# Kernel tuning notes

Hardware: AMD Instinct MI355X
Metric: run time of the kernel (lower is better)

The kernel has to match this reference:

```python
import jax, jax.numpy as jnp
import numpy as np


def setup_inputs() -> dict:
    key = jax.random.key(0)
    k0, k1, k2, k3, k4, k5 = jax.random.split(key, 6)
    L1, L2, B, D = 512, 512, 32, 1024
    inputs1 = jax.random.normal(k0, (L1, B, D), dtype=jnp.float32)
    inputs2 = jax.random.normal(k1, (L2, B, D), dtype=jnp.float32)
    # mask value 0 marks a valid token (module keeps pairs where both masks == 0)
    mask1 = jax.random.randint(k2, (L1, B), 0, 2, dtype=jnp.int64)
    mask2 = jax.random.randint(k3, (L2, B), 0, 2, dtype=jnp.int64)
    W = jax.random.normal(k4, (D, D), dtype=jnp.float32) * 0.02
    b = jax.random.normal(k5, (1,), dtype=jnp.float32) * 0.02
    return {"inputs1": inputs1, "inputs2": inputs2, "mask1": mask1,
            "mask2": mask2, "W": W, "b": b, "k": 256}


def reference(inputs1, inputs2, mask1, mask2, W, b, k):
    # inputs: [len, bsz, hdim]; masks: [len, bsz]
    H1 = jnp.transpose(inputs1, (1, 0, 2))  # [B, L1, D]
    H2 = jnp.transpose(inputs2, (1, 0, 2))  # [B, L2, D]
    # bilinear scores: H1 @ W @ H2^T + b, then relu  -> [B, L1, L2]
    S = jax.nn.relu(jnp.einsum('bid,de,bje->bij', H1, W, H2) + b[0])
    # pair is valid iff both mask entries are 0
    valid = (mask1.T[:, :, None] == 0) & (mask2.T[:, None, :] == 0)  # [B, L1, L2]
    B = S.shape[0]
    S_flat = jnp.where(valid.reshape(B, -1), S.reshape(B, -1), -jnp.inf)
    num_elems = S_flat.shape[1]
    k_actual = min(k, num_elems)
    q, _ = jax.lax.top_k(S_flat, k_actual)  # [B, k_actual]
    # replace -inf tail entries with the last finite value in each row
    neg = jnp.isneginf(q)
    q_num_finite = k_actual - neg.sum(axis=-1)  # [B]
    fill = jnp.take_along_axis(q, (q_num_finite - 1)[:, None], axis=1)  # [B, 1]
    q = jnp.where(neg, fill, q)
    if k_actual < k:
        q = jnp.concatenate(
            [q, jnp.broadcast_to(q[:, -1:], (B, k - k_actual))], axis=1)
    return q
```

## Files before the change

kernel.cpp:

```cpp
#include <hip/hip_runtime.h>

typedef __bf16 bf16_t;
typedef bf16_t bf16x8 __attribute__((ext_vector_type(8)));
typedef float floatx4 __attribute__((ext_vector_type(4)));

#define L1C 512
#define L2C 512
#define BC  32
#define DC  1024
#define KTOP 256
#define NBIN 4096
#define CAP  1024
#define FBUF 16384

__device__ __forceinline__ unsigned short f2bf(float f) {
    unsigned u = __float_as_uint(f);
    u += 0x7FFFu + ((u >> 16) & 1u);
    return (unsigned short)(u >> 16);
}

__device__ __forceinline__ void g2l16(const unsigned short* g, unsigned short* l) {
    __builtin_amdgcn_global_load_lds((const unsigned int*)g, (unsigned int*)l,
                                     16, 0, 0);
}

__device__ __forceinline__ float decode_key(unsigned k) {
    return __uint_as_float(k & 0x7FFFFFFFu);
}

__global__ __launch_bounds__(512) void scan_kernel(
    const int* __restrict__ mask1, const int* __restrict__ mask2,
    int* __restrict__ idx1, int* __restrict__ idx2,
    unsigned* __restrict__ nv1, unsigned* __restrict__ nv2,
    unsigned* __restrict__ cnt) {
    __shared__ unsigned sc[512];
    int b = blockIdx.x, t = threadIdx.x;
    for (int which = 0; which < 2; which++) {
        const int* m = which ? mask2 : mask1;
        int* idx = which ? idx2 : idx1;
        unsigned v = (m[t * BC + b] == 0) ? 1u : 0u;
        sc[t] = v;
        __syncthreads();
        for (int off = 1; off < 512; off <<= 1) {
            unsigned x = (t >= off) ? sc[t - off] : 0u;
            __syncthreads();
            sc[t] += x;
            __syncthreads();
        }
        if (v) idx[b * 512 + sc[t] - 1] = t;
        if (t == 511) { if (which) nv2[b] = sc[511]; else nv1[b] = sc[511]; }
        __syncthreads();
    }
    if (t < 16) cnt[b * 16 + t] = 0;
}

__global__ __launch_bounds__(256) void prep_kernel(
    const float* __restrict__ in1, const float* __restrict__ in2,
    const float* __restrict__ W,
    const int* __restrict__ idx1, const int* __restrict__ idx2,
    const unsigned* __restrict__ nv1, const unsigned* __restrict__ nv2,
    unsigned short* __restrict__ A1c, unsigned short* __restrict__ A2c,
    unsigned short* __restrict__ Wb) {
    int r = blockIdx.x, t = threadIdx.x;
    const float* src;
    unsigned short* dst;
    if (r < 2 * 16384) {
        int which = r >> 14;
        int rr = r & 16383;
        int b = rr >> 9, vi = rr & 511;
        unsigned nv = which ? nv2[b] : nv1[b];
        unsigned pad = (nv + 127u) & ~127u;
        if ((unsigned)vi >= pad) return;
        dst = (which ? A2c : A1c) + ((size_t)b * 512 + vi) * DC;
        if ((unsigned)vi < nv) {
            int l = (which ? idx2 : idx1)[b * 512 + vi];
            src = (which ? in2 : in1) + (size_t)(l * BC + b) * DC;
        } else {
            ushort4 z = {0, 0, 0, 0};
            reinterpret_cast<ushort4*>(dst)[t] = z;
            return;
        }
    } else {
        int r3 = r - 2 * 16384;
        src = W + (size_t)r3 * DC;
        dst = Wb + (size_t)r3 * DC;
    }
    float4 v = reinterpret_cast<const float4*>(src)[t];
    ushort4 o;
    o.x = f2bf(v.x); o.y = f2bf(v.y); o.z = f2bf(v.z); o.w = f2bf(v.w);
    reinterpret_cast<ushort4*>(dst)[t] = o;
}

__global__ __launch_bounds__(256) void gemm1_kernel(
    const unsigned short* __restrict__ A,
    const unsigned short* __restrict__ Bt,
    unsigned short* __restrict__ C,
    const unsigned* __restrict__ nv2) {
    int bi = blockIdx.x >> 2, mt = blockIdx.x & 3;
    unsigned pad2 = (nv2[bi] + 127u) & ~127u;
    if ((unsigned)(mt * 128) >= pad2) return;
    __shared__ unsigned short As[128][32];
    __shared__ unsigned short Bs[128][32];
    int tid = threadIdx.x;
    int wave = tid >> 6, lane = tid & 63;
    int lane15 = lane & 15, quad = lane >> 4;
    int wm = wave >> 1, wn = wave & 1;
    size_t m0 = (size_t)bi * 512 + mt * 128;
    size_t n0 = (size_t)blockIdx.y * 128;

    floatx4 zero = {0.f, 0.f, 0.f, 0.f};
    floatx4 acc[4][4];
#pragma unroll
    for (int i = 0; i < 4; i++)
#pragma unroll
        for (int j = 0; j < 4; j++) acc[i][j] = zero;

    for (int k0 = 0; k0 < DC; k0 += 32) {
#pragma unroll
        for (int c = 0; c < 2; c++) {
            int cid = c * 256 + tid;
            int row = cid >> 2, col8 = (cid & 3) * 8;
            unsigned short* lbase = &As[0][0] + (c * 256 + wave * 64) * 8;
            g2l16(&A[(m0 + row) * DC + k0 + col8], lbase);
            unsigned short* lbase2 = &Bs[0][0] + (c * 256 + wave * 64) * 8;
            g2l16(&Bt[(n0 + row) * DC + k0 + col8], lbase2);
        }
        __syncthreads();
        bf16x8 af[4], bfr[4];
#pragma unroll
        for (int mi = 0; mi < 4; mi++)
            af[mi] = *reinterpret_cast<const bf16x8*>(&As[wm * 64 + mi * 16 + lane15][quad * 8]);
#pragma unroll
        for (int ni = 0; ni < 4; ni++)
            bfr[ni] = *reinterpret_cast<const bf16x8*>(&Bs[wn * 64 + ni * 16 + lane15][quad * 8]);
#pragma unroll
        for (int mi = 0; mi < 4; mi++)
#pragma unroll
            for (int ni = 0; ni < 4; ni++)
                acc[mi][ni] = __builtin_amdgcn_mfma_f32_16x16x32_bf16(
                    af[mi], bfr[ni], acc[mi][ni], 0, 0, 0);
        __syncthreads();
    }
#pragma unroll
    for (int mi = 0; mi < 4; mi++)
#pragma unroll
        for (int ni = 0; ni < 4; ni++)
#pragma unroll
            for (int r = 0; r < 4; r++) {
                size_t row = m0 + wm * 64 + mi * 16 + quad * 4 + r;
                size_t col = n0 + wn * 64 + ni * 16 + lane15;
                C[row * DC + col] = f2bf(acc[mi][ni][r]);
            }
}

__global__ __launch_bounds__(256) void gemm2_kernel(
    const unsigned short* __restrict__ A1c,
    const unsigned short* __restrict__ V,
    const unsigned* __restrict__ nv1, const unsigned* __restrict__ nv2,
    const float* __restrict__ bptr,
    unsigned* __restrict__ cand,
    unsigned* __restrict__ cnt) {
    int L = blockIdx.x;
    int xcd = L & 7, tile = (L >> 3) & 15, chunk = L >> 7;
    int b = xcd + (chunk << 3);
    int bx = tile & 3, by = tile >> 2;
    int m0 = bx * 128, n0 = by * 128;
    int gblk = b * 16 + by * 4 + bx;
    int tid = threadIdx.x;
    unsigned nv1v = nv1[b], nv2v = nv2[b];
    unsigned pad1 = (nv1v + 127u) & ~127u, pad2 = (nv2v + 127u) & ~127u;
    if ((unsigned)m0 >= pad1 || (unsigned)n0 >= pad2) {
        if (tid == 0) cnt[gblk] = 0;
        return;
    }
    __shared__ unsigned short As[128][32];
    __shared__ unsigned short Bs[128][32];
    __shared__ unsigned lh[NBIN];
    __shared__ unsigned csum[256];
    __shared__ unsigned tsh, lcnt, zeq;
    int wave = tid >> 6, lane = tid & 63;
    int lane15 = lane & 15, quad = lane >> 4;
    int wm = wave >> 1, wn = wave & 1;
    const unsigned short* Ab = A1c + (size_t)b * 512 * DC;
    const unsigned short* Bb = V + (size_t)b * 512 * DC;

    for (int i = tid; i < NBIN; i += 256) lh[i] = 0;

    floatx4 zero = {0.f, 0.f, 0.f, 0.f};
    floatx4 acc[4][4];
#pragma unroll
    for (int i = 0; i < 4; i++)
#pragma unroll
        for (int j = 0; j < 4; j++) acc[i][j] = zero;

    for (int k0 = 0; k0 < DC; k0 += 32) {
#pragma unroll
        for (int c = 0; c < 2; c++) {
            int cid = c * 256 + tid;
            int row = cid >> 2, col8 = (cid & 3) * 8;
            unsigned short* lbase = &As[0][0] + (c * 256 + wave * 64) * 8;
            g2l16(&Ab[(size_t)(m0 + row) * DC + k0 + col8], lbase);
            unsigned short* lbase2 = &Bs[0][0] + (c * 256 + wave * 64) * 8;
            g2l16(&Bb[(size_t)(n0 + row) * DC + k0 + col8], lbase2);
        }
        __syncthreads();
        bf16x8 af[4], bfr[4];
#pragma unroll
        for (int mi = 0; mi < 4; mi++)
            af[mi] = *reinterpret_cast<const bf16x8*>(&As[wm * 64 + mi * 16 + lane15][quad * 8]);
#pragma unroll
        for (int ni = 0; ni < 4; ni++)
            bfr[ni] = *reinterpret_cast<const bf16x8*>(&Bs[wn * 64 + ni * 16 + lane15][quad * 8]);
#pragma unroll
        for (int mi = 0; mi < 4; mi++)
#pragma unroll
            for (int ni = 0; ni < 4; ni++)
                acc[mi][ni] = __builtin_amdgcn_mfma_f32_16x16x32_bf16(
                    af[mi], bfr[ni], acc[mi][ni], 0, 0, 0);
        __syncthreads();
    }

    float bias = bptr[0];
    unsigned zc = 0;
#pragma unroll
    for (int ni = 0; ni < 4; ni++) {
        int jl = n0 + wn * 64 + ni * 16 + lane15;
        int v2 = (unsigned)jl < nv2v;
#pragma unroll
        for (int mi = 0; mi < 4; mi++)
#pragma unroll
            for (int r = 0; r < 4; r++) {
                int il = m0 + wm * 64 + mi * 16 + quad * 4 + r;
                float s = acc[mi][ni][r] + bias;
                if (v2 && (unsigned)il < nv1v) {
                    if (s > 0.f)
                        atomicAdd(&lh[(__float_as_uint(s) | 0x80000000u) >> 20], 1u);
                    else
                        zc++;
                }
            }
    }
    if (zc) atomicAdd(&lh[2048], zc);
    __syncthreads();
    unsigned s16 = 0;
#pragma unroll
    for (int i = 0; i < 16; i++) s16 += lh[tid * 16 + i];
    csum[tid] = s16;
    __syncthreads();
    if (tid == 0) {
        unsigned cum = 0, bin = 2048;
        int found = 0;
        for (int c = 255; c >= 128 && !found; --c) {
            unsigned cs = csum[c];
            if (cum + cs >= KTOP) {
                for (int bb = c * 16 + 15; bb >= c * 16; --bb) {
                    unsigned h = lh[bb];
                    if (cum + h >= KTOP) { bin = (unsigned)bb; found = 1; break; }
                    cum += h;
                }
            } else cum += cs;
        }
        tsh = bin << 20;
        lcnt = 0;
        zeq = 0;
    }
    __syncthreads();
    unsigned T = tsh;
    unsigned base = (unsigned)gblk * CAP;
#pragma unroll
    for (int ni = 0; ni < 4; ni++) {
        int jl = n0 + wn * 64 + ni * 16 + lane15;
        int v2 = (unsigned)jl < nv2v;
#pragma unroll
        for (int mi = 0; mi < 4; mi++)
#pragma unroll
            for (int r = 0; r < 4; r++) {
                int il = m0 + wm * 64 + mi * 16 + quad * 4 + r;
                float s = acc[mi][ni][r] + bias;
                s = s > 0.f ? s : 0.f;
                unsigned key = (v2 && (unsigned)il < nv1v)
                                   ? (__float_as_uint(s) | 0x80000000u) : 0u;
                if (key > T) {
                    unsigned p = atomicAdd(&lcnt, 1u);
                    if (p < CAP) cand[base + p] = key;
                } else if (key == T) {
                    unsigned z = atomicAdd(&zeq, 1u);
                    if (z < KTOP) {
                        unsigned p = atomicAdd(&lcnt, 1u);
                        if (p < CAP) cand[base + p] = key;
                    }
                }
            }
    }
    __syncthreads();
    if (tid == 0) cnt[gblk] = lcnt < CAP ? lcnt : CAP;
}

__global__ __launch_bounds__(1024) void final_kernel(
    const unsigned* __restrict__ cand, const unsigned* __restrict__ cnt,
    float* __restrict__ out) {
    __shared__ unsigned buf[FBUF];
    __shared__ unsigned h[NBIN];
    __shared__ unsigned ss[256];
    __shared__ unsigned scnt_s[16], off_s[16];
    __shared__ unsigned ntot_s, sel_c, sel_a, B_s, R_s, mcount;
    __shared__ int have_s;
    __shared__ unsigned srt[256];
    int b = blockIdx.x, tid = threadIdx.x;
    int wv = tid >> 6, ln = tid & 63;

    if (tid < 16) {
        unsigned c = cnt[b * 16 + tid];
        scnt_s[tid] = c < CAP ? c : CAP;
    }
    __syncthreads();
    if (tid == 0) {
        unsigned o = 0;
        for (int i = 0; i < 16; i++) { off_s[i] = o; o += scnt_s[i]; }
        ntot_s = o;
        have_s = 1;
    }
    __syncthreads();
    {
        unsigned c = scnt_s[wv], o = off_s[wv];
        const unsigned* p = cand + (size_t)(b * 16 + wv) * CAP;
        for (unsigned i = ln; i < c; i += 64) buf[o + i] = p[i];
    }
    __syncthreads();
    unsigned n = ntot_s;

    unsigned Kr = KTOP;
    unsigned pfx = 0;
    unsigned kth = 0;
    for (int pass = 0; pass < 3; pass++) {
        int bins = (pass < 2) ? NBIN : 256;
        int shift = (pass == 0) ? 20 : (pass == 1) ? 8 : 0;
        int nch = bins >> 4;
        for (int i = tid; i < bins; i += 1024) h[i] = 0;
        __syncthreads();
        for (unsigned i = tid; i < n; i += 1024) {
            unsigned k = buf[i];
            bool ok = (pass == 0) ||
                      (pass == 1 && (k >> 20) == pfx) ||
                      (pass == 2 && (k >> 8) == pfx);
            if (ok) atomicAdd(&h[(k >> shift) & (bins - 1)], 1u);
        }
        __syncthreads();
        if (tid < nch) {
            unsigned s = 0;
#pragma unroll
            for (int i = 0; i < 16; i++) s += h[tid * 16 + i];
            ss[tid] = s;
        }
        __syncthreads();
        for (int off = 1; off < nch; off <<= 1) {
            unsigned v = 0;
            if (tid < nch && tid + (unsigned)off < (unsigned)nch) v = ss[tid + off];
            __syncthreads();
            if (tid < nch) ss[tid] += v;
            __syncthreads();
        }
        if (pass == 0) {
            if (tid == 0) have_s = (ss[0] >= KTOP);
            __syncthreads();
            if (!have_s) break;
        }
        if (tid < nch) {
            unsigned above = (tid + 1 < (unsigned)nch) ? ss[tid + 1] : 0u;
            if (above < Kr && ss[tid] >= Kr) { sel_c = tid; sel_a = above; }
        }
        __syncthreads();
        if (tid == 0) {
            unsigned cum = sel_a;
            for (int bb = (int)sel_c * 16 + 15; bb >= (int)sel_c * 16; --bb) {
                unsigned hb = h[bb];
                if (cum + hb >= Kr) { B_s = (unsigned)bb; R_s = Kr - cum; break; }
                cum += hb;
            }
        }
        __syncthreads();
        unsigned Bv = B_s;
        Kr = R_s;
        if (pass == 0) pfx = Bv;
        else if (pass == 1) pfx = (pfx << 12) | Bv;
        else kth = (pfx << 8) | Bv;
        __syncthreads();
    }

    if (tid == 0) mcount = 0;
    __syncthreads();
    int have = have_s;
    unsigned lim = have ? kth : 0u;
    for (unsigned i = tid; i < n; i += 1024) {
        unsigned k = buf[i];
        if (k > lim) {
            unsigned p = atomicAdd(&mcount, 1u);
            if (p < 256) srt[p] = k;
        }
    }
    __syncthreads();
    unsigned m = mcount;
    if (tid < 256 && tid >= (int)m) srt[tid] = have ? kth : 0u;
    for (int k2 = 2; k2 <= 256; k2 <<= 1) {
        for (int j2 = k2 >> 1; j2 > 0; j2 >>= 1) {
            __syncthreads();
            if (tid < 256) {
                int ixj = tid ^ j2;
                if (ixj > tid) {
                    unsigned a = srt[tid], c = srt[ixj];
                    bool up = (tid & k2) == 0;
                    if (up ? (a < c) : (a > c)) { srt[tid] = c; srt[ixj] = a; }
                }
            }
        }
    }
    __syncthreads();
    if (tid < 256) {
        unsigned nval = have ? KTOP : (m < KTOP ? m : KTOP);
        float v;
        if ((unsigned)tid < nval) v = decode_key(srt[tid]);
        else v = (nval > 0) ? decode_key(srt[nval - 1]) : -__builtin_inff();
        out[b * KTOP + tid] = v;
    }
}

extern "C" void kernel_launch(void* const* d_in, const int* in_sizes, int n_in,
                              void* d_out, int out_size, void* d_ws, size_t ws_size,
                              hipStream_t stream) {
    const float* in1   = (const float*)d_in[0];
    const float* in2   = (const float*)d_in[1];
    const int*   mask1 = (const int*)d_in[2];
    const int*   mask2 = (const int*)d_in[3];
    const float* W     = (const float*)d_in[4];
    const float* bias  = (const float*)d_in[5];
    float* out = (float*)d_out;

    char* ws = (char*)d_ws;
    size_t off = 0;
    const size_t nElem = (size_t)512 * BC * DC;
    unsigned short* A1c = (unsigned short*)(ws + off); off += nElem * 2;
    unsigned short* A2c = (unsigned short*)(ws + off); off += nElem * 2;
    unsigned short* Wb  = (unsigned short*)(ws + off); off += (size_t)DC * DC * 2;
    unsigned short* V   = (unsigned short*)(ws + off); off += nElem * 2;
    unsigned* cand = (unsigned*)(ws + off); off += (size_t)BC * 16 * CAP * 4;
    unsigned* cnt  = (unsigned*)(ws + off); off += (size_t)BC * 16 * 4;
    int* idx1 = (int*)(ws + off); off += (size_t)BC * 512 * 4;
    int* idx2 = (int*)(ws + off); off += (size_t)BC * 512 * 4;
    unsigned* nv1 = (unsigned*)(ws + off); off += BC * 4;
    unsigned* nv2 = (unsigned*)(ws + off); off += BC * 4;

    scan_kernel<<<BC, 512, 0, stream>>>(mask1, mask2, idx1, idx2, nv1, nv2, cnt);
    prep_kernel<<<2 * 16384 + 1024, 256, 0, stream>>>(
        in1, in2, W, idx1, idx2, nv1, nv2, A1c, A2c, Wb);
    gemm1_kernel<<<dim3(128, 8), 256, 0, stream>>>(A2c, Wb, V, nv2);
    gemm2_kernel<<<512, 256, 0, stream>>>(A1c, V, nv1, nv2, bias, cand, cnt);
    final_kernel<<<BC, 1024, 0, stream>>>(cand, cnt, out);
}
```

Baseline: 263.2 us.

## Shrink GEMM tiles to 64 rows and pad valid tokens to 64

Both GEMMs now use smaller tiles: 64x128 in gemm1 and 64x64 in gemm2. Valid-token padding drops from 128 to 64, which wastes less compute on padded rows and launches more blocks, so occupancy rises and the CU load is more even. gemm2 now emits 64 candidate segments per batch with a smaller cap. Its per-block threshold search uses a parallel suffix scan instead of a serial thread-0 loop, and final_kernel clamps the total candidate count to its buffer. Smaller tiles lower data reuse per MFMA and mean more histogram clears and per-block overhead.

```diff
diff --git a/kernel.cpp b/kernel.cpp
--- a/kernel.cpp
+++ b/kernel.cpp
@@ -10,7 +10,8 @@
 #define DC  1024
 #define KTOP 256
 #define NBIN 4096
-#define CAP  1024
+#define CAP  512
+#define NT   64
 #define FBUF 16384
 
 __device__ __forceinline__ unsigned short f2bf(float f) {
@@ -51,7 +52,7 @@
         if (t == 511) { if (which) nv2[b] = sc[511]; else nv1[b] = sc[511]; }
         __syncthreads();
     }
-    if (t < 16) cnt[b * 16 + t] = 0;
+    if (t < NT) cnt[b * NT + t] = 0;
 }
 
 __global__ __launch_bounds__(256) void prep_kernel(
@@ -69,7 +70,7 @@
         int rr = r & 16383;
         int b = rr >> 9, vi = rr & 511;
         unsigned nv = which ? nv2[b] : nv1[b];
-        unsigned pad = (nv + 127u) & ~127u;
+        unsigned pad = (nv + 63u) & ~63u;
         if ((unsigned)vi >= pad) return;
         dst = (which ? A2c : A1c) + ((size_t)b * 512 + vi) * DC;
         if ((unsigned)vi < nv) {
@@ -96,47 +97,50 @@
     const unsigned short* __restrict__ Bt,
     unsigned short* __restrict__ C,
     const unsigned* __restrict__ nv2) {
-    int bi = blockIdx.x >> 2, mt = blockIdx.x & 3;
-    unsigned pad2 = (nv2[bi] + 127u) & ~127u;
-    if ((unsigned)(mt * 128) >= pad2) return;
-    __shared__ unsigned short As[128][32];
+    int bi = blockIdx.x >> 3, mt = blockIdx.x & 7;
+    unsigned pad2 = (nv2[bi] + 63u) & ~63u;
+    if ((unsigned)(mt * 64) >= pad2) return;
+    __shared__ unsigned short As[64][32];
     __shared__ unsigned short Bs[128][32];
     int tid = threadIdx.x;
     int wave = tid >> 6, lane = tid & 63;
     int lane15 = lane & 15, quad = lane >> 4;
-    int wm = wave >> 1, wn = wave & 1;
-    size_t m0 = (size_t)bi * 512 + mt * 128;
+    size_t m0 = (size_t)bi * 512 + mt * 64;
     size_t n0 = (size_t)blockIdx.y * 128;
 
     floatx4 zero = {0.f, 0.f, 0.f, 0.f};
-    floatx4 acc[4][4];
+    floatx4 acc[4][2];
 #pragma unroll
     for (int i = 0; i < 4; i++)
 #pragma unroll
-        for (int j = 0; j < 4; j++) acc[i][j] = zero;
+        for (int j = 0; j < 2; j++) acc[i][j] = zero;
 
     for (int k0 = 0; k0 < DC; k0 += 32) {
+        {
+            int row = tid >> 2, col8 = (tid & 3) * 8;
+            g2l16(&A[(m0 + row) * DC + k0 + col8],
+                  &As[0][0] + (wave * 64) * 8);
+        }
 #pragma unroll
         for (int c = 0; c < 2; c++) {
-            int cid = c * 256 + tid;
-            int row = cid >> 2, col8 = (cid & 3) * 8;
-            unsigned short* lbase = &As[0][0] + (c * 256 + wave * 64) * 8;
-            g2l16(&A[(m0 + row) * DC + k0 + col8], lbase);
-            unsigned short* lbase2 = &Bs[0][0] + (c * 256 + wave * 64) * 8;
-            g2l16(&Bt[(n0 + row) * DC + k0 + col8], lbase2);
-        }
-        __syncthreads();
-        bf16x8 af[4], bfr[4];
+            int cid2 = c * 256 + tid;
+            int row = cid2 >> 2, col8 = (cid2 & 3) * 8;
+            g2l16(&Bt[(n0 + row) * DC + k0 + col8],
+                  &Bs[0][0] + (c * 256 + wave * 64) * 8);
+        }
+        __syncthreads();
+        bf16x8 af[4], bfr[2];
 #pragma unroll
         for (int mi = 0; mi < 4; mi++)
-            af[mi] = *reinterpret_cast<const bf16x8*>(&As[wm * 64 + mi * 16 + lane15][quad * 8]);
-#pragma unroll
-        for (int ni = 0; ni < 4; ni++)
-            bfr[ni] = *reinterpret_cast<const bf16x8*>(&Bs[wn * 64 + ni * 16 + lane15][quad * 8]);
+            af[mi] = *reinterpret_cast<const bf16x8*>(&As[mi * 16 + lane15][quad * 8]);
+#pragma unroll
+        for (int ni = 0; ni < 2; ni++)
+            bfr[ni] = *reinterpret_cast<const bf16x8*>(
+                &Bs[wave * 32 + ni * 16 + lane15][quad * 8]);
 #pragma unroll
         for (int mi = 0; mi < 4; mi++)
 #pragma unroll
-            for (int ni = 0; ni < 4; ni++)
+            for (int ni = 0; ni < 2; ni++)
                 acc[mi][ni] = __builtin_amdgcn_mfma_f32_16x16x32_bf16(
                     af[mi], bfr[ni], acc[mi][ni], 0, 0, 0);
         __syncthreads();
@@ -144,11 +148,11 @@
 #pragma unroll
     for (int mi = 0; mi < 4; mi++)
 #pragma unroll
-        for (int ni = 0; ni < 4; ni++)
+        for (int ni = 0; ni < 2; ni++)
 #pragma unroll
             for (int r = 0; r < 4; r++) {
-                size_t row = m0 + wm * 64 + mi * 16 + quad * 4 + r;
-                size_t col = n0 + wn * 64 + ni * 16 + lane15;
+                size_t row = m0 + mi * 16 + quad * 4 + r;
+                size_t col = n0 + wave * 32 + ni * 16 + lane15;
                 C[row * DC + col] = f2bf(acc[mi][ni][r]);
             }
 }
@@ -161,62 +165,52 @@
     unsigned* __restrict__ cand,
     unsigned* __restrict__ cnt) {
     int L = blockIdx.x;
-    int xcd = L & 7, tile = (L >> 3) & 15, chunk = L >> 7;
+    int xcd = L & 7, tile = (L >> 3) & 63, chunk = L >> 9;
     int b = xcd + (chunk << 3);
-    int bx = tile & 3, by = tile >> 2;
-    int m0 = bx * 128, n0 = by * 128;
-    int gblk = b * 16 + by * 4 + bx;
+    int tx = tile & 7, ty = tile >> 3;
+    int m0 = ty * 64, n0 = tx * 64;
+    int gblk = b * NT + tile;
     int tid = threadIdx.x;
     unsigned nv1v = nv1[b], nv2v = nv2[b];
-    unsigned pad1 = (nv1v + 127u) & ~127u, pad2 = (nv2v + 127u) & ~127u;
+    unsigned pad1 = (nv1v + 63u) & ~63u, pad2 = (nv2v + 63u) & ~63u;
     if ((unsigned)m0 >= pad1 || (unsigned)n0 >= pad2) {
         if (tid == 0) cnt[gblk] = 0;
         return;
     }
-    __shared__ unsigned short As[128][32];
-    __shared__ unsigned short Bs[128][32];
+    __shared__ unsigned short As[64][32];
+    __shared__ unsigned short Bs[64][32];
     __shared__ unsigned lh[NBIN];
     __shared__ unsigned csum[256];
-    __shared__ unsigned tsh, lcnt, zeq;
+    __shared__ unsigned sel_c, sel_a, tsh, lcnt, zeq;
     int wave = tid >> 6, lane = tid & 63;
     int lane15 = lane & 15, quad = lane >> 4;
-    int wm = wave >> 1, wn = wave & 1;
     const unsigned short* Ab = A1c + (size_t)b * 512 * DC;
     const unsigned short* Bb = V + (size_t)b * 512 * DC;
 
     for (int i = tid; i < NBIN; i += 256) lh[i] = 0;
+    if (tid == 0) { sel_c = 0xFFFFFFFFu; lcnt = 0; zeq = 0; }
 
     floatx4 zero = {0.f, 0.f, 0.f, 0.f};
-    floatx4 acc[4][4];
-#pragma unroll
-    for (int i = 0; i < 4; i++)
-#pragma unroll
-        for (int j = 0; j < 4; j++) acc[i][j] = zero;
+    floatx4 acc[4];
+#pragma unroll
+    for (int i = 0; i < 4; i++) acc[i] = zero;
 
     for (int k0 = 0; k0 < DC; k0 += 32) {
-#pragma unroll
-        for (int c = 0; c < 2; c++) {
-            int cid = c * 256 + tid;
-            int row = cid >> 2, col8 = (cid & 3) * 8;
-            unsigned short* lbase = &As[0][0] + (c * 256 + wave * 64) * 8;
-            g2l16(&Ab[(size_t)(m0 + row) * DC + k0 + col8], lbase);
-            unsigned short* lbase2 = &Bs[0][0] + (c * 256 + wave * 64) * 8;
-            g2l16(&Bb[(size_t)(n0 + row) * DC + k0 + col8], lbase2);
-        }
-        __syncthreads();
-        bf16x8 af[4], bfr[4];
-#pragma unroll
-        for (int mi = 0; mi < 4; mi++)
-            af[mi] = *reinterpret_cast<const bf16x8*>(&As[wm * 64 + mi * 16 + lane15][quad * 8]);
+        int row = tid >> 2, col8 = (tid & 3) * 8;
+        g2l16(&Ab[(size_t)(m0 + row) * DC + k0 + col8],
+              &As[0][0] + (wave * 64) * 8);
+        g2l16(&Bb[(size_t)(n0 + row) * DC + k0 + col8],
+              &Bs[0][0] + (wave * 64) * 8);
+        __syncthreads();
+        bf16x8 af, bfr[4];
+        af = *reinterpret_cast<const bf16x8*>(&As[wave * 16 + lane15][quad * 8]);
 #pragma unroll
         for (int ni = 0; ni < 4; ni++)
-            bfr[ni] = *reinterpret_cast<const bf16x8*>(&Bs[wn * 64 + ni * 16 + lane15][quad * 8]);
-#pragma unroll
-        for (int mi = 0; mi < 4; mi++)
-#pragma unroll
-            for (int ni = 0; ni < 4; ni++)
-                acc[mi][ni] = __builtin_amdgcn_mfma_f32_16x16x32_bf16(
-                    af[mi], bfr[ni], acc[mi][ni], 0, 0, 0);
+            bfr[ni] = *reinterpret_cast<const bf16x8*>(&Bs[ni * 16 + lane15][quad * 8]);
+#pragma unroll
+        for (int ni = 0; ni < 4; ni++)
+            acc[ni] = __builtin_amdgcn_mfma_f32_16x16x32_bf16(
+                af, bfr[ni], acc[ni], 0, 0, 0);
         __syncthreads();
     }
 
@@ -224,21 +218,19 @@
     unsigned zc = 0;
 #pragma unroll
     for (int ni = 0; ni < 4; ni++) {
-        int jl = n0 + wn * 64 + ni * 16 + lane15;
+        int jl = n0 + ni * 16 + lane15;
         int v2 = (unsigned)jl < nv2v;
 #pragma unroll
-        for (int mi = 0; mi < 4; mi++)
-#pragma unroll
-            for (int r = 0; r < 4; r++) {
-                int il = m0 + wm * 64 + mi * 16 + quad * 4 + r;
-                float s = acc[mi][ni][r] + bias;
-                if (v2 && (unsigned)il < nv1v) {
-                    if (s > 0.f)
-                        atomicAdd(&lh[(__float_as_uint(s) | 0x80000000u) >> 20], 1u);
-                    else
-                        zc++;
-                }
-            }
+        for (int r = 0; r < 4; r++) {
+            int il = m0 + wave * 16 + quad * 4 + r;
+            float s = acc[ni][r] + bias;
+            if (v2 && (unsigned)il < nv1v) {
+                if (s > 0.f)
+                    atomicAdd(&lh[(__float_as_uint(s) | 0x80000000u) >> 20], 1u);
+                else
+                    zc++;
+            }
+        }
     }
     if (zc) atomicAdd(&lh[2048], zc);
     __syncthreads();
@@ -247,50 +239,57 @@
     for (int i = 0; i < 16; i++) s16 += lh[tid * 16 + i];
     csum[tid] = s16;
     __syncthreads();
+    for (int off = 1; off < 256; off <<= 1) {
+        unsigned v = (tid + off < 256) ? csum[tid + off] : 0u;
+        __syncthreads();
+        csum[tid] += v;
+        __syncthreads();
+    }
+    {
+        unsigned above = (tid < 255) ? csum[tid + 1] : 0u;
+        if (tid >= 128 && csum[tid] >= KTOP && above < KTOP) {
+            sel_c = (unsigned)tid; sel_a = above;
+        }
+    }
+    __syncthreads();
     if (tid == 0) {
-        unsigned cum = 0, bin = 2048;
-        int found = 0;
-        for (int c = 255; c >= 128 && !found; --c) {
-            unsigned cs = csum[c];
-            if (cum + cs >= KTOP) {
-                for (int bb = c * 16 + 15; bb >= c * 16; --bb) {
-                    unsigned h = lh[bb];
-                    if (cum + h >= KTOP) { bin = (unsigned)bb; found = 1; break; }
-                    cum += h;
-                }
-            } else cum += cs;
-        }
-        tsh = bin << 20;
-        lcnt = 0;
-        zeq = 0;
+        if (sel_c == 0xFFFFFFFFu) {
+            tsh = 2048u << 20;
+        } else {
+            unsigned cum = sel_a, bin = 2048;
+            for (int bb = (int)sel_c * 16 + 15; bb >= (int)sel_c * 16; --bb) {
+                unsigned hb = lh[bb];
+                if (cum + hb >= KTOP) { bin = (unsigned)bb; break; }
+                cum += hb;
+            }
+            tsh = bin << 20;
+        }
     }
     __syncthreads();
     unsigned T = tsh;
     unsigned base = (unsigned)gblk * CAP;
 #pragma unroll
     for (int ni = 0; ni < 4; ni++) {
-        int jl = n0 + wn * 64 + ni * 16 + lane15;
+        int jl = n0 + ni * 16 + lane15;
         int v2 = (unsigned)jl < nv2v;
 #pragma unroll
-        for (int mi = 0; mi < 4; mi++)
-#pragma unroll
-            for (int r = 0; r < 4; r++) {
-                int il = m0 + wm * 64 + mi * 16 + quad * 4 + r;
-                float s = acc[mi][ni][r] + bias;
-                s = s > 0.f ? s : 0.f;
-                unsigned key = (v2 && (unsigned)il < nv1v)
-                                   ? (__float_as_uint(s) | 0x80000000u) : 0u;
-                if (key > T) {
+        for (int r = 0; r < 4; r++) {
+            int il = m0 + wave * 16 + quad * 4 + r;
+            float s = acc[ni][r] + bias;
+            s = s > 0.f ? s : 0.f;
+            unsigned key = (v2 && (unsigned)il < nv1v)
+                               ? (__float_as_uint(s) | 0x80000000u) : 0u;
+            if (key > T) {
+                unsigned p = atomicAdd(&lcnt, 1u);
+                if (p < CAP) cand[base + p] = key;
+            } else if (key == T) {
+                unsigned z = atomicAdd(&zeq, 1u);
+                if (z < KTOP) {
                     unsigned p = atomicAdd(&lcnt, 1u);
                     if (p < CAP) cand[base + p] = key;
-                } else if (key == T) {
-                    unsigned z = atomicAdd(&zeq, 1u);
-                    if (z < KTOP) {
-                        unsigned p = atomicAdd(&lcnt, 1u);
-                        if (p < CAP) cand[base + p] = key;
-                    }
                 }
             }
+        }
     }
     __syncthreads();
     if (tid == 0) cnt[gblk] = lcnt < CAP ? lcnt : CAP;
@@ -302,28 +301,34 @@
     __shared__ unsigned buf[FBUF];
     __shared__ unsigned h[NBIN];
     __shared__ unsigned ss[256];
-    __shared__ unsigned scnt_s[16], off_s[16];
+    __shared__ unsigned scnt_s[NT], off_s[NT];
     __shared__ unsigned ntot_s, sel_c, sel_a, B_s, R_s, mcount;
     __shared__ int have_s;
     __shared__ unsigned srt[256];
     int b = blockIdx.x, tid = threadIdx.x;
     int wv = tid >> 6, ln = tid & 63;
 
-    if (tid < 16) {
-        unsigned c = cnt[b * 16 + tid];
+    if (tid < NT) {
+        unsigned c = cnt[b * NT + tid];
         scnt_s[tid] = c < CAP ? c : CAP;
     }
     __syncthreads();
     if (tid == 0) {
         unsigned o = 0;
-        for (int i = 0; i < 16; i++) { off_s[i] = o; o += scnt_s[i]; }
+        for (int i = 0; i < NT; i++) {
+            unsigned c = scnt_s[i];
+            if (o + c > FBUF) c = (o < FBUF) ? FBUF - o : 0;
+            scnt_s[i] = c;
+            off_s[i] = o;
+            o += c;
+        }
         ntot_s = o;
         have_s = 1;
     }
     __syncthreads();
-    {
-        unsigned c = scnt_s[wv], o = off_s[wv];
-        const unsigned* p = cand + (size_t)(b * 16 + wv) * CAP;
+    for (int s = wv; s < NT; s += 16) {
+        unsigned c = scnt_s[s], o = off_s[s];
+        const unsigned* p = cand + (size_t)(b * NT + s) * CAP;
         for (unsigned i = ln; i < c; i += 64) buf[o + i] = p[i];
     }
     __syncthreads();
@@ -442,8 +447,8 @@
     unsigned short* A2c = (unsigned short*)(ws + off); off += nElem * 2;
     unsigned short* Wb  = (unsigned short*)(ws + off); off += (size_t)DC * DC * 2;
     unsigned short* V   = (unsigned short*)(ws + off); off += nElem * 2;
-    unsigned* cand = (unsigned*)(ws + off); off += (size_t)BC * 16 * CAP * 4;
-    unsigned* cnt  = (unsigned*)(ws + off); off += (size_t)BC * 16 * 4;
+    unsigned* cand = (unsigned*)(ws + off); off += (size_t)BC * NT * CAP * 4;
+    unsigned* cnt  = (unsigned*)(ws + off); off += (size_t)BC * NT * 4;
     int* idx1 = (int*)(ws + off); off += (size_t)BC * 512 * 4;
     int* idx2 = (int*)(ws + off); off += (size_t)BC * 512 * 4;
     unsigned* nv1 = (unsigned*)(ws + off); off += BC * 4;
@@ -452,7 +457,7 @@
     scan_kernel<<<BC, 512, 0, stream>>>(mask1, mask2, idx1, idx2, nv1, nv2, cnt);
     prep_kernel<<<2 * 16384 + 1024, 256, 0, stream>>>(
         in1, in2, W, idx1, idx2, nv1, nv2, A1c, A2c, Wb);
-    gemm1_kernel<<<dim3(128, 8), 256, 0, stream>>>(A2c, Wb, V, nv2);
-    gemm2_kernel<<<512, 256, 0, stream>>>(A1c, V, nv1, nv2, bias, cand, cnt);
+    gemm1_kernel<<<dim3(256, 8), 256, 0, stream>>>(A2c, Wb, V, nv2);
+    gemm2_kernel<<<2048, 256, 0, stream>>>(A1c, V, nv1, nv2, bias, cand, cnt);
     final_kernel<<<BC, 1024, 0, stream>>>(cand, cnt, out);
 }
```

Result: no change. 262.1 us (-0.4%).
